# Kernel tuning notes

Hardware: AMD Instinct MI355X
Metric: run time of the kernel (lower is better)

Reference implementation:

```python
import jax, jax.numpy as jnp
import numpy as np

HIDDEN = 512
HEADS = 8
D_HEAD = HIDDEN // HEADS
SCALE = D_HEAD ** -0.5
LN_EPS = 1e-5
N_L = 2048
N_R = 4096


def setup_inputs() -> dict:
    key = jax.random.key(0)
    ks = jax.random.split(key, 10)
    s = HIDDEN ** -0.5
    return {
        "q": jax.random.normal(ks[0], (N_L, HIDDEN), jnp.float32),
        "kv": jax.random.normal(ks[1], (N_R, HIDDEN), jnp.float32),
        "bias": jax.random.normal(ks[2], (N_L, N_R), jnp.float32),
        "Wq": jax.random.normal(ks[3], (HIDDEN, HIDDEN), jnp.float32) * s,
        "Wk": jax.random.normal(ks[4], (HIDDEN, HIDDEN), jnp.float32) * s,
        "Wv": jax.random.normal(ks[5], (HIDDEN, HIDDEN), jnp.float32) * s,
        "Wo": jax.random.normal(ks[6], (HIDDEN, HIDDEN), jnp.float32) * s,
        "bo": jnp.zeros((HIDDEN,), jnp.float32),
        "gamma": jnp.ones((HIDDEN,), jnp.float32),
        "beta": jnp.zeros((HIDDEN,), jnp.float32),
    }


def reference(q, kv, bias, Wq, Wk, Wv, Wo, bo, gamma, beta):
    # projections (torch Linear: x @ W.T)
    Q = (q @ Wq.T).reshape(N_L, HEADS, D_HEAD).transpose(1, 0, 2)   # [h, N_L, d]
    K = (kv @ Wk.T).reshape(N_R, HEADS, D_HEAD).transpose(1, 0, 2)  # [h, N_R, d]
    V = (kv @ Wv.T).reshape(N_R, HEADS, D_HEAD).transpose(1, 0, 2)  # [h, N_R, d]
    logits = SCALE * jnp.einsum('hld,hrd->hlr', Q, K) + bias[None]  # [h, N_L, N_R]
    attn = jax.nn.softmax(logits, axis=-1)                          # dropout p=0 -> identity
    ctx = jnp.einsum('hlr,hrd->hld', attn, V)                       # [h, N_L, d]
    ctx = ctx.transpose(1, 0, 2).reshape(N_L, HIDDEN)
    out = ctx @ Wo.T + bo
    x = out + q
    mu = jnp.mean(x, axis=-1, keepdims=True)
    var = jnp.mean((x - mu) ** 2, axis=-1, keepdims=True)
    out = (x - mu) * jax.lax.rsqrt(var + LN_EPS) * gamma + beta
    attn_mean = attn.mean(axis=0)                                   # [N_L, N_R]
    return out, attn_mean
```

## Files before the change

kernel.cpp:

```cpp
#include <hip/hip_runtime.h>
#include <hip/hip_bf16.h>
#include <stdint.h>

#define NL 2048
#define NR 4096
#define NCHUNK 8
#define CHUNK (NR / NCHUNK)
#define SCALE 0.125f
#define LN_EPS 1e-5f

typedef __attribute__((ext_vector_type(8))) short short8;
typedef __attribute__((ext_vector_type(4))) float float4v;

static __device__ __forceinline__ short f2bf(float f) {
  union { float f; uint32_t u; } v; v.f = f;
  uint32_t u = v.u;
  uint32_t r = (u + 0x7FFFu + ((u >> 16) & 1u)) >> 16;
  return (short)(r & 0xFFFFu);
}
static __device__ __forceinline__ float bf2f(short b) {
  union { uint32_t u; float f; } v; v.u = ((uint32_t)(uint16_t)b) << 16;
  return v.f;
}
static __device__ __forceinline__ uint32_t cvtpk(float a, float b) {
  uint32_t r;
  asm("v_cvt_pk_bf16_f32 %0, %1, %2" : "=v"(r) : "v"(a), "v"(b));
  return r;
}

__global__ void k0_cvt(const float* __restrict__ q, const float* __restrict__ kv,
                       const float* __restrict__ Wq, const float* __restrict__ Wk,
                       const float* __restrict__ Wv, const float* __restrict__ Wo,
                       short* __restrict__ qb, short* __restrict__ kvb,
                       short* __restrict__ Wqb, short* __restrict__ Wkb,
                       short* __restrict__ Wvb, short* __restrict__ Wob) {
  int i = blockIdx.x * blockDim.x + threadIdx.x;
  const float* src; short* dst;
  if (i < 131072)                 { src = q;  dst = qb;  }
  else if ((i -= 131072) < 262144){ src = kv; dst = kvb; }
  else if ((i -= 262144) < 32768) { src = Wq; dst = Wqb; }
  else if ((i -= 32768) < 32768)  { src = Wk; dst = Wkb; }
  else if ((i -= 32768) < 32768)  { src = Wv; dst = Wvb; }
  else { i -= 32768;                src = Wo; dst = Wob; }
  const float4* s4 = reinterpret_cast<const float4*>(src) + (size_t)i * 2;
  float4 a = s4[0], b = s4[1];
  short8 o;
  o[0] = f2bf(a.x); o[1] = f2bf(a.y); o[2] = f2bf(a.z); o[3] = f2bf(a.w);
  o[4] = f2bf(b.x); o[5] = f2bf(b.y); o[6] = f2bf(b.z); o[7] = f2bf(b.w);
  *reinterpret_cast<short8*>(dst + (size_t)i * 8) = o;
}

__global__ void k1_proj(const short* __restrict__ qb, const short* __restrict__ kvb,
                        const short* __restrict__ Wqb, const short* __restrict__ Wkb,
                        const short* __restrict__ Wvb,
                        short* __restrict__ Qb, short* __restrict__ Kb,
                        short* __restrict__ VT) {
  int lane = threadIdx.x & 63, warp = threadIdx.x >> 6;
  int wid = blockIdx.x * 4 + warp;
  int lr = lane & 15, lg = lane >> 4;
  const short *src, *W; short* dst; int mt, ct, mode;
  if (wid < 1024)      { src = qb;  W = Wqb; dst = Qb; mt = wid & 127; ct = wid >> 7; mode = 0; }
  else if (wid < 3072) { int id = wid - 1024; src = kvb; W = Wkb; dst = Kb; mt = id & 255; ct = id >> 8; mode = 0; }
  else                 { int id = wid - 3072; src = kvb; W = Wvb; dst = VT; mt = id & 255; ct = id >> 8; mode = 1; }
  int m0 = mt * 16, c0 = ct * 64;
  float4v acc[4] = {};
  const short* arow = src + (m0 + lr) * 512 + 8 * lg;
#pragma unroll
  for (int kk = 0; kk < 16; ++kk) {
    short8 a = *reinterpret_cast<const short8*>(arow + kk * 32);
#pragma unroll
    for (int cs = 0; cs < 4; ++cs) {
      const short* bp = W + (c0 + cs * 16 + lr) * 512 + kk * 32 + 8 * lg;
      short8 b = *reinterpret_cast<const short8*>(bp);
      acc[cs] = __builtin_amdgcn_mfma_f32_16x16x32_bf16(a, b, acc[cs], 0, 0, 0);
    }
  }
  if (mode == 0) {
#pragma unroll
    for (int cs = 0; cs < 4; ++cs)
#pragma unroll
      for (int j = 0; j < 4; ++j)
        dst[(m0 + 4 * lg + j) * 512 + c0 + cs * 16 + lr] = f2bf(acc[cs][j]);
  } else {
#pragma unroll
    for (int cs = 0; cs < 4; ++cs)
#pragma unroll
      for (int j = 0; j < 4; ++j)
        dst[(c0 + cs * 16 + lr) * 4096 + m0 + 4 * lg + j] = f2bf(acc[cs][j]);
  }
}

#define K2_LOADB(dst, itv)                                                    \
  {                                                                           \
    int r0n = r_base + (itv) * 32;                                            \
    _Pragma("unroll") for (int s = 0; s < 2; ++s)                             \
    _Pragma("unroll") for (int j = 0; j < 4; ++j)                             \
      dst[s][j] = bias[(l0 + 4 * lg + j) * (size_t)NR + r0n + s * 16 + lr];   \
  }
#define K2_BODY(bv, itv)                                                      \
  {                                                                           \
    int r0 = r_base + (itv) * 32;                                             \
    float4v cc[2];                                                            \
    _Pragma("unroll") for (int s = 0; s < 2; ++s) {                           \
      const short* kp = Kb + (r0 + s * 16 + lr) * 512 + w * 64 + 8 * lg;      \
      short8 b0 = *reinterpret_cast<const short8*>(kp);                       \
      short8 b1 = *reinterpret_cast<const short8*>(kp + 32);                  \
      float4v c = {};                                                         \
      c = __builtin_amdgcn_mfma_f32_16x16x32_bf16(qa0, b0, c, 0, 0, 0);       \
      c = __builtin_amdgcn_mfma_f32_16x16x32_bf16(qa1, b1, c, 0, 0, 0);       \
      cc[s] = c;                                                              \
    }                                                                         \
    _Pragma("unroll") for (int s = 0; s < 2; ++s)                             \
    _Pragma("unroll") for (int j = 0; j < 4; ++j)                             \
      sums[j] += __expf(fmaf(SCALE, cc[s][j], bv[s][j]));                     \
  }
__global__ void __launch_bounds__(512, 8)
k2_passA(const short* __restrict__ Qb, const short* __restrict__ Kb,
         const float* __restrict__ bias, float* __restrict__ S_part) {
  int lane = threadIdx.x & 63, w = threadIdx.x >> 6;
  int lr = lane & 15, lg = lane >> 4;
  int l0 = blockIdx.x * 16;
  int chunk = blockIdx.y;
  int r_base = chunk * CHUNK;
  float sums[4] = {};
  const short* qrow = Qb + (l0 + lr) * 512 + 8 * lg;
  short8 qa0 = *reinterpret_cast<const short8*>(qrow + w * 64);
  short8 qa1 = *reinterpret_cast<const short8*>(qrow + w * 64 + 32);
  float bvA[2][4], bvB[2][4];
  K2_LOADB(bvA, 0)
#pragma unroll 1
  for (int it2 = 0; it2 < 8; ++it2) {
    K2_LOADB(bvB, 2 * it2 + 1)
    K2_BODY(bvA, 2 * it2)
    if (it2 < 7) K2_LOADB(bvA, 2 * it2 + 2)
    K2_BODY(bvB, 2 * it2 + 1)
  }
#pragma unroll
  for (int j = 0; j < 4; ++j) {
    float v = sums[j];
    v += __shfl_xor(v, 1, 64); v += __shfl_xor(v, 2, 64);
    v += __shfl_xor(v, 4, 64); v += __shfl_xor(v, 8, 64);
    sums[j] = v;
  }
  if (lr == 0) {
#pragma unroll
    for (int j = 0; j < 4; ++j)
      S_part[(chunk * 8 + w) * NL + l0 + 4 * lg + j] = sums[j];
  }
}

__global__ void k2b_reduceS(const float* __restrict__ S_part, float* __restrict__ Sinv) {
  int i = blockIdx.x * blockDim.x + threadIdx.x;
  int h = i >> 11, l = i & 2047;
  float s = 0.f;
#pragma unroll
  for (int c = 0; c < NCHUNK; ++c) s += S_part[(c * 8 + h) * NL + l];
  Sinv[i] = 1.0f / s;
}

__global__ void __launch_bounds__(512, 8)
k3_passB(const short* __restrict__ Qb, const short* __restrict__ Kb,
         const short* __restrict__ VT, const float* __restrict__ bias,
         const float* __restrict__ Sinv,
         float* __restrict__ attn_mean, short* __restrict__ ctx_part) {
  __shared__ __align__(16) short P[8][2][16][40];
  __shared__ float BIAS[2][16][33];
  int t = threadIdx.x;
  int lane = t & 63, w = t >> 6;
  int lr = lane & 15, lg = lane >> 4;
  int l0 = blockIdx.x * 16;
  int chunk = blockIdx.y;
  int r_base = chunk * CHUNK;
  float4v acc[4] = {};
  float sinv = Sinv[w * NL + l0 + lr];
  const short* qrow = Qb + (l0 + lr) * 512 + 8 * lg;
  short8 qa0 = *reinterpret_cast<const short8*>(qrow + w * 64);
  short8 qa1 = *reinterpret_cast<const short8*>(qrow + w * 64 + 32);
  int sq = t >> 5, sr = t & 31;
  BIAS[0][sq][sr] = bias[(l0 + sq) * (size_t)NR + r_base + sr];
  __syncthreads();
#pragma unroll 1
  for (int it = 0; it < CHUNK / 32; ++it) {
    int cb = it & 1;
    int r0 = r_base + it * 32;
    if (it < CHUNK / 32 - 1)
      BIAS[cb ^ 1][sq][sr] = bias[(l0 + sq) * (size_t)NR + r0 + 32 + sr];
#pragma unroll
    for (int s = 0; s < 2; ++s) {
      const short* kp = Kb + (r0 + s * 16 + lr) * 512 + w * 64 + 8 * lg;
      short8 b0 = *reinterpret_cast<const short8*>(kp);
      short8 b1 = *reinterpret_cast<const short8*>(kp + 32);
      float4v c = {};
      c = __builtin_amdgcn_mfma_f32_16x16x32_bf16(b0, qa0, c, 0, 0, 0);
      c = __builtin_amdgcn_mfma_f32_16x16x32_bf16(b1, qa1, c, 0, 0, 0);
      float e0 = __expf(fmaf(SCALE, c[0], BIAS[cb][lr][s * 16 + 4 * lg + 0])) * sinv;
      float e1 = __expf(fmaf(SCALE, c[1], BIAS[cb][lr][s * 16 + 4 * lg + 1])) * sinv;
      float e2 = __expf(fmaf(SCALE, c[2], BIAS[cb][lr][s * 16 + 4 * lg + 2])) * sinv;
      float e3 = __expf(fmaf(SCALE, c[3], BIAS[cb][lr][s * 16 + 4 * lg + 3])) * sinv;
      uint2 pk; pk.x = cvtpk(e0, e1); pk.y = cvtpk(e2, e3);
      *reinterpret_cast<uint2*>(&P[w][cb][lr][s * 16 + 4 * lg]) = pk;
    }
    short8 pa = *reinterpret_cast<const short8*>(&P[w][cb][lr][8 * lg]);
#pragma unroll
    for (int ds = 0; ds < 4; ++ds) {
      const short* vp = VT + (w * 64 + ds * 16 + lr) * 4096 + r0 + 8 * lg;
      short8 vb = *reinterpret_cast<const short8*>(vp);
      acc[ds] = __builtin_amdgcn_mfma_f32_16x16x32_bf16(pa, vb, acc[ds], 0, 0, 0);
    }
    __syncthreads();
    {
      float v = 0.f;
#pragma unroll
      for (int hh = 0; hh < 8; ++hh) v += bf2f(P[hh][cb][sq][sr]);
      attn_mean[(size_t)(l0 + sq) * NR + r0 + sr] = v * 0.125f;
    }
  }
#pragma unroll
  for (int ds = 0; ds < 4; ++ds)
#pragma unroll
    for (int j = 0; j < 4; ++j)
      ctx_part[(chunk * NL + l0 + 4 * lg + j) * 512 + w * 64 + ds * 16 + lr] =
          f2bf(acc[ds][j]);
}

__global__ void k4pre(const short* __restrict__ ctx_part, short* __restrict__ ctxsum) {
  int i = blockIdx.x * blockDim.x + threadIdx.x;
  float sm[8] = {};
#pragma unroll
  for (int c = 0; c < NCHUNK; ++c) {
    short8 v = *reinterpret_cast<const short8*>(ctx_part + (size_t)c * NL * 512 + (size_t)i * 8);
#pragma unroll
    for (int u = 0; u < 8; ++u) sm[u] += bf2f(v[u]);
  }
  short8 o;
#pragma unroll
  for (int u = 0; u < 8; ++u) o[u] = f2bf(sm[u]);
  *reinterpret_cast<short8*>(ctxsum + (size_t)i * 8) = o;
}

__global__ void k4_out(const short* __restrict__ ctxsum, const short* __restrict__ Wob,
                       const float* __restrict__ q, const float* __restrict__ bo,
                       const float* __restrict__ gamma, const float* __restrict__ beta,
                       float* __restrict__ out) {
  __shared__ float xs[16][512];
  int lane = threadIdx.x & 63, warp = threadIdx.x >> 6;
  int lr = lane & 15, lg = lane >> 4;
  int l0 = blockIdx.x * 16;
  short8 afr[16];
#pragma unroll
  for (int kk = 0; kk < 16; ++kk)
    afr[kk] = *reinterpret_cast<const short8*>(ctxsum + (l0 + lr) * 512 + kk * 32 + 8 * lg);
#pragma unroll 1
  for (int cs = 0; cs < 8; ++cs) {
    int col0 = warp * 128 + cs * 16;
    float4v c = {};
#pragma unroll
    for (int kk = 0; kk < 16; ++kk) {
      const short* bp = Wob + (col0 + lr) * 512 + kk * 32 + 8 * lg;
      short8 b = *reinterpret_cast<const short8*>(bp);
      c = __builtin_amdgcn_mfma_f32_16x16x32_bf16(afr[kk], b, c, 0, 0, 0);
    }
#pragma unroll
    for (int j = 0; j < 4; ++j) {
      int row = l0 + 4 * lg + j, col = col0 + lr;
      xs[4 * lg + j][col] = c[j] + bo[col] + q[row * 512 + col];
    }
  }
  __syncthreads();
  int tid = threadIdx.x;
  int rl = tid >> 4, g = tid & 15;
  float sum = 0.f;
#pragma unroll
  for (int i = 0; i < 32; ++i) sum += xs[rl][g + 16 * i];
  sum += __shfl_xor(sum, 1, 64); sum += __shfl_xor(sum, 2, 64);
  sum += __shfl_xor(sum, 4, 64); sum += __shfl_xor(sum, 8, 64);
  float mu = sum * (1.0f / 512.0f);
  float vs = 0.f;
#pragma unroll
  for (int i = 0; i < 32; ++i) { float d = xs[rl][g + 16 * i] - mu; vs += d * d; }
  vs += __shfl_xor(vs, 1, 64); vs += __shfl_xor(vs, 2, 64);
  vs += __shfl_xor(vs, 4, 64); vs += __shfl_xor(vs, 8, 64);
  float rs = rsqrtf(vs * (1.0f / 512.0f) + LN_EPS);
#pragma unroll
  for (int i = 0; i < 32; ++i) {
    int cc = g + 16 * i;
    out[(l0 + rl) * 512 + cc] = (xs[rl][cc] - mu) * rs * gamma[cc] + beta[cc];
  }
}

extern "C" void kernel_launch(void* const* d_in, const int* in_sizes, int n_in,
                              void* d_out, int out_size, void* d_ws, size_t ws_size,
                              hipStream_t stream) {
  const float* q     = (const float*)d_in[0];
  const float* kv    = (const float*)d_in[1];
  const float* bias  = (const float*)d_in[2];
  const float* Wq    = (const float*)d_in[3];
  const float* Wk    = (const float*)d_in[4];
  const float* Wv    = (const float*)d_in[5];
  const float* Wo    = (const float*)d_in[6];
  const float* bo    = (const float*)d_in[7];
  const float* gamma = (const float*)d_in[8];
  const float* beta  = (const float*)d_in[9];
  float* out = (float*)d_out;
  float* attn_mean = out + (size_t)NL * 512;

  char* ws = (char*)d_ws;
  short* qb       = (short*)(ws + 0);
  short* kvb      = (short*)(ws + 2097152);
  short* Wqb      = (short*)(ws + 6291456);
  short* Wkb      = (short*)(ws + 6815744);
  short* Wvb      = (short*)(ws + 7340032);
  short* Wob      = (short*)(ws + 7864320);
  short* Qb       = (short*)(ws + 8388608);
  short* Kb       = (short*)(ws + 10485760);
  short* VT       = (short*)(ws + 14680064);
  float* S_part   = (float*)(ws + 18874368);
  float* Sinv     = (float*)(ws + 19398656);
  short* ctx_part = (short*)(ws + 19464192);
  short* ctxsum   = (short*)(ws + 36241408);

  k0_cvt<<<2048, 256, 0, stream>>>(q, kv, Wq, Wk, Wv, Wo, qb, kvb, Wqb, Wkb, Wvb, Wob);
  k1_proj<<<1280, 256, 0, stream>>>(qb, kvb, Wqb, Wkb, Wvb, Qb, Kb, VT);
  k2_passA<<<dim3(128, 8), 512, 0, stream>>>(Qb, Kb, bias, S_part);
  k2b_reduceS<<<64, 256, 0, stream>>>(S_part, Sinv);
  k3_passB<<<dim3(128, 8), 512, 0, stream>>>(Qb, Kb, VT, bias, Sinv, attn_mean, ctx_part);
  k4pre<<<512, 256, 0, stream>>>(ctx_part, ctxsum);
  k4_out<<<128, 256, 0, stream>>>(ctxsum, Wob, q, bo, gamma, beta, out);
}
```

Before: 373.8 us.

## Vectorize bias loads, batch P tiles per barrier, widen attn_mean stores

Pass A and pass B now read bias directly from global memory as float4 in the MFMA output layout, using the transposed K-by-Q product. This replaces the shared-memory bias staging and the scalar loads. Pass B processes four 32-column subtiles before each block barrier, using a wider P buffer, and writes attn_mean as float4 vectors, so there are fewer syncs and fewer narrow stores. Launch bounds for pass B drop to 4 blocks per CU because of the larger LDS footprint, which can lower occupancy.

```diff
diff --git a/kernel.cpp b/kernel.cpp
--- a/kernel.cpp
+++ b/kernel.cpp
@@ -8,6 +8,7 @@
 #define CHUNK (NR / NCHUNK)
 #define SCALE 0.125f
 #define LN_EPS 1e-5f
+#define GRP 4
 
 typedef __attribute__((ext_vector_type(8))) short short8;
 typedef __attribute__((ext_vector_type(4))) float float4v;
@@ -20,6 +21,10 @@
 }
 static __device__ __forceinline__ float bf2f(short b) {
   union { uint32_t u; float f; } v; v.u = ((uint32_t)(uint16_t)b) << 16;
+  return v.f;
+}
+static __device__ __forceinline__ float bfu2f(uint32_t lo16) {
+  union { uint32_t u; float f; } v; v.u = lo16 << 16;
   return v.f;
 }
 static __device__ __forceinline__ uint32_t cvtpk(float a, float b) {
@@ -90,30 +95,6 @@
   }
 }
 
-#define K2_LOADB(dst, itv)                                                    \
-  {                                                                           \
-    int r0n = r_base + (itv) * 32;                                            \
-    _Pragma("unroll") for (int s = 0; s < 2; ++s)                             \
-    _Pragma("unroll") for (int j = 0; j < 4; ++j)                             \
-      dst[s][j] = bias[(l0 + 4 * lg + j) * (size_t)NR + r0n + s * 16 + lr];   \
-  }
-#define K2_BODY(bv, itv)                                                      \
-  {                                                                           \
-    int r0 = r_base + (itv) * 32;                                             \
-    float4v cc[2];                                                            \
-    _Pragma("unroll") for (int s = 0; s < 2; ++s) {                           \
-      const short* kp = Kb + (r0 + s * 16 + lr) * 512 + w * 64 + 8 * lg;      \
-      short8 b0 = *reinterpret_cast<const short8*>(kp);                       \
-      short8 b1 = *reinterpret_cast<const short8*>(kp + 32);                  \
-      float4v c = {};                                                         \
-      c = __builtin_amdgcn_mfma_f32_16x16x32_bf16(qa0, b0, c, 0, 0, 0);       \
-      c = __builtin_amdgcn_mfma_f32_16x16x32_bf16(qa1, b1, c, 0, 0, 0);       \
-      cc[s] = c;                                                              \
-    }                                                                         \
-    _Pragma("unroll") for (int s = 0; s < 2; ++s)                             \
-    _Pragma("unroll") for (int j = 0; j < 4; ++j)                             \
-      sums[j] += __expf(fmaf(SCALE, cc[s][j], bv[s][j]));                     \
-  }
 __global__ void __launch_bounds__(512, 8)
 k2_passA(const short* __restrict__ Qb, const short* __restrict__ Kb,
          const float* __restrict__ bias, float* __restrict__ S_part) {
@@ -122,31 +103,33 @@
   int l0 = blockIdx.x * 16;
   int chunk = blockIdx.y;
   int r_base = chunk * CHUNK;
-  float sums[4] = {};
+  float sum = 0.f;
   const short* qrow = Qb + (l0 + lr) * 512 + 8 * lg;
   short8 qa0 = *reinterpret_cast<const short8*>(qrow + w * 64);
   short8 qa1 = *reinterpret_cast<const short8*>(qrow + w * 64 + 32);
-  float bvA[2][4], bvB[2][4];
-  K2_LOADB(bvA, 0)
-#pragma unroll 1
-  for (int it2 = 0; it2 < 8; ++it2) {
-    K2_LOADB(bvB, 2 * it2 + 1)
-    K2_BODY(bvA, 2 * it2)
-    if (it2 < 7) K2_LOADB(bvA, 2 * it2 + 2)
-    K2_BODY(bvB, 2 * it2 + 1)
-  }
-#pragma unroll
-  for (int j = 0; j < 4; ++j) {
-    float v = sums[j];
-    v += __shfl_xor(v, 1, 64); v += __shfl_xor(v, 2, 64);
-    v += __shfl_xor(v, 4, 64); v += __shfl_xor(v, 8, 64);
-    sums[j] = v;
-  }
-  if (lr == 0) {
-#pragma unroll
-    for (int j = 0; j < 4; ++j)
-      S_part[(chunk * 8 + w) * NL + l0 + 4 * lg + j] = sums[j];
-  }
+#pragma unroll 4
+  for (int it = 0; it < 16; ++it) {
+    int r0 = r_base + it * 32;
+#pragma unroll
+    for (int s = 0; s < 2; ++s) {
+      float4 bv = *reinterpret_cast<const float4*>(
+          &bias[(size_t)(l0 + lr) * NR + r0 + s * 16 + 4 * lg]);
+      const short* kp = Kb + (r0 + s * 16 + lr) * 512 + w * 64 + 8 * lg;
+      short8 b0 = *reinterpret_cast<const short8*>(kp);
+      short8 b1 = *reinterpret_cast<const short8*>(kp + 32);
+      float4v c = {};
+      c = __builtin_amdgcn_mfma_f32_16x16x32_bf16(b0, qa0, c, 0, 0, 0);
+      c = __builtin_amdgcn_mfma_f32_16x16x32_bf16(b1, qa1, c, 0, 0, 0);
+      sum += __expf(fmaf(SCALE, c[0], bv.x));
+      sum += __expf(fmaf(SCALE, c[1], bv.y));
+      sum += __expf(fmaf(SCALE, c[2], bv.z));
+      sum += __expf(fmaf(SCALE, c[3], bv.w));
+    }
+  }
+  sum += __shfl_xor(sum, 16, 64);
+  sum += __shfl_xor(sum, 32, 64);
+  if (lane < 16)
+    S_part[(chunk * 8 + w) * NL + l0 + lane] = sum;
 }
 
 __global__ void k2b_reduceS(const float* __restrict__ S_part, float* __restrict__ Sinv) {
@@ -158,13 +141,12 @@
   Sinv[i] = 1.0f / s;
 }
 
-__global__ void __launch_bounds__(512, 8)
+__global__ void __launch_bounds__(512, 4)
 k3_passB(const short* __restrict__ Qb, const short* __restrict__ Kb,
          const short* __restrict__ VT, const float* __restrict__ bias,
          const float* __restrict__ Sinv,
          float* __restrict__ attn_mean, short* __restrict__ ctx_part) {
-  __shared__ __align__(16) short P[8][2][16][40];
-  __shared__ float BIAS[2][16][33];
+  __shared__ __align__(16) short P[8][2][16][136];
   int t = threadIdx.x;
   int lane = t & 63, w = t >> 6;
   int lr = lane & 15, lg = lane >> 4;
@@ -176,43 +158,51 @@
   const short* qrow = Qb + (l0 + lr) * 512 + 8 * lg;
   short8 qa0 = *reinterpret_cast<const short8*>(qrow + w * 64);
   short8 qa1 = *reinterpret_cast<const short8*>(qrow + w * 64 + 32);
-  int sq = t >> 5, sr = t & 31;
-  BIAS[0][sq][sr] = bias[(l0 + sq) * (size_t)NR + r_base + sr];
-  __syncthreads();
+  int mrow = t >> 5, mc0 = (t & 31) * 4;
 #pragma unroll 1
-  for (int it = 0; it < CHUNK / 32; ++it) {
-    int cb = it & 1;
-    int r0 = r_base + it * 32;
-    if (it < CHUNK / 32 - 1)
-      BIAS[cb ^ 1][sq][sr] = bias[(l0 + sq) * (size_t)NR + r0 + 32 + sr];
-#pragma unroll
-    for (int s = 0; s < 2; ++s) {
-      const short* kp = Kb + (r0 + s * 16 + lr) * 512 + w * 64 + 8 * lg;
-      short8 b0 = *reinterpret_cast<const short8*>(kp);
-      short8 b1 = *reinterpret_cast<const short8*>(kp + 32);
-      float4v c = {};
-      c = __builtin_amdgcn_mfma_f32_16x16x32_bf16(b0, qa0, c, 0, 0, 0);
-      c = __builtin_amdgcn_mfma_f32_16x16x32_bf16(b1, qa1, c, 0, 0, 0);
-      float e0 = __expf(fmaf(SCALE, c[0], BIAS[cb][lr][s * 16 + 4 * lg + 0])) * sinv;
-      float e1 = __expf(fmaf(SCALE, c[1], BIAS[cb][lr][s * 16 + 4 * lg + 1])) * sinv;
-      float e2 = __expf(fmaf(SCALE, c[2], BIAS[cb][lr][s * 16 + 4 * lg + 2])) * sinv;
-      float e3 = __expf(fmaf(SCALE, c[3], BIAS[cb][lr][s * 16 + 4 * lg + 3])) * sinv;
-      uint2 pk; pk.x = cvtpk(e0, e1); pk.y = cvtpk(e2, e3);
-      *reinterpret_cast<uint2*>(&P[w][cb][lr][s * 16 + 4 * lg]) = pk;
-    }
-    short8 pa = *reinterpret_cast<const short8*>(&P[w][cb][lr][8 * lg]);
-#pragma unroll
-    for (int ds = 0; ds < 4; ++ds) {
-      const short* vp = VT + (w * 64 + ds * 16 + lr) * 4096 + r0 + 8 * lg;
-      short8 vb = *reinterpret_cast<const short8*>(vp);
-      acc[ds] = __builtin_amdgcn_mfma_f32_16x16x32_bf16(pa, vb, acc[ds], 0, 0, 0);
+  for (int g = 0; g < CHUNK / (32 * GRP); ++g) {
+    int cb = g & 1;
+    int rg = r_base + g * 32 * GRP;
+#pragma unroll
+    for (int u = 0; u < GRP; ++u) {
+      int r0 = rg + u * 32;
+#pragma unroll
+      for (int s = 0; s < 2; ++s) {
+        float4 bv = *reinterpret_cast<const float4*>(
+            &bias[(size_t)(l0 + lr) * NR + r0 + s * 16 + 4 * lg]);
+        const short* kp = Kb + (r0 + s * 16 + lr) * 512 + w * 64 + 8 * lg;
+        short8 b0 = *reinterpret_cast<const short8*>(kp);
+        short8 b1 = *reinterpret_cast<const short8*>(kp + 32);
+        float4v c = {};
+        c = __builtin_amdgcn_mfma_f32_16x16x32_bf16(b0, qa0, c, 0, 0, 0);
+        c = __builtin_amdgcn_mfma_f32_16x16x32_bf16(b1, qa1, c, 0, 0, 0);
+        float e0 = __expf(fmaf(SCALE, c[0], bv.x)) * sinv;
+        float e1 = __expf(fmaf(SCALE, c[1], bv.y)) * sinv;
+        float e2 = __expf(fmaf(SCALE, c[2], bv.z)) * sinv;
+        float e3 = __expf(fmaf(SCALE, c[3], bv.w)) * sinv;
+        uint2 pk; pk.x = cvtpk(e0, e1); pk.y = cvtpk(e2, e3);
+        *reinterpret_cast<uint2*>(&P[w][cb][lr][u * 32 + s * 16 + 4 * lg]) = pk;
+      }
+      short8 pa = *reinterpret_cast<const short8*>(&P[w][cb][lr][u * 32 + 8 * lg]);
+#pragma unroll
+      for (int ds = 0; ds < 4; ++ds) {
+        const short* vp = VT + (w * 64 + ds * 16 + lr) * 4096 + r0 + 8 * lg;
+        short8 vb = *reinterpret_cast<const short8*>(vp);
+        acc[ds] = __builtin_amdgcn_mfma_f32_16x16x32_bf16(pa, vb, acc[ds], 0, 0, 0);
+      }
     }
     __syncthreads();
     {
-      float v = 0.f;
-#pragma unroll
-      for (int hh = 0; hh < 8; ++hh) v += bf2f(P[hh][cb][sq][sr]);
-      attn_mean[(size_t)(l0 + sq) * NR + r0 + sr] = v * 0.125f;
+      float v0 = 0.f, v1 = 0.f, v2 = 0.f, v3 = 0.f;
+#pragma unroll
+      for (int hh = 0; hh < 8; ++hh) {
+        uint2 p8 = *reinterpret_cast<const uint2*>(&P[hh][cb][mrow][mc0]);
+        v0 += bfu2f(p8.x & 0xFFFFu); v1 += bfu2f(p8.x >> 16);
+        v2 += bfu2f(p8.y & 0xFFFFu); v3 += bfu2f(p8.y >> 16);
+      }
+      float4 o; o.x = v0 * 0.125f; o.y = v1 * 0.125f;
+      o.z = v2 * 0.125f; o.w = v3 * 0.125f;
+      *reinterpret_cast<float4*>(&attn_mean[(size_t)(l0 + mrow) * NR + rg + mc0]) = o;
     }
   }
 #pragma unroll
```

Result: slower. 412.5 us (+10.4%).
